# Kernel tuning notes

Hardware: AMD Instinct MI355X
Metric: run time of the kernel (lower is better)

Reference implementation:

```python
import jax, jax.numpy as jnp
from jax import lax
import numpy as np


def _conv2d(x, w, b, pad):
    # x: NCHW, w: OIHW
    o = lax.conv_general_dilated(x, w, window_strides=(1, 1),
                                 padding=[(pad, pad), (pad, pad)],
                                 dimension_numbers=('NCHW', 'OIHW', 'NCHW'))
    return o + b[None, :, None, None]


def _maxpool(x, kh, kw):
    return lax.reduce_window(x, -jnp.inf, lax.max,
                             window_dimensions=(1, 1, kh, kw),
                             window_strides=(1, 1, kh, kw),
                             padding='VALID')


def _l2norm(x, axis):
    n = jnp.sqrt(jnp.sum(x * x, axis=axis, keepdims=True))
    return x / jnp.maximum(n, 1e-12)


def setup_inputs() -> dict:
    key = jax.random.key(0)
    ks = jax.random.split(key, 12)
    d = {}
    d['x'] = jax.random.normal(ks[0], (16, 128, 40, 200), dtype=jnp.float32)
    d['cluster_centers'] = jax.random.uniform(ks[1], (64, 128), dtype=jnp.float32)
    d['conv_w'] = jax.random.normal(ks[2], (64, 128, 1, 1), dtype=jnp.float32) * 0.05
    d['conv_b'] = jax.random.normal(ks[3], (64,), dtype=jnp.float32) * 0.05
    d['w1'] = jax.random.normal(ks[4], (256, 128, 5, 5), dtype=jnp.float32) * 0.02
    d['b1'] = jax.random.normal(ks[5], (256,), dtype=jnp.float32) * 0.02
    d['w2'] = jax.random.normal(ks[6], (512, 256, 5, 5), dtype=jnp.float32) * 0.02
    d['b2'] = jax.random.normal(ks[7], (512,), dtype=jnp.float32) * 0.02
    d['w3'] = jax.random.normal(ks[8], (1024, 512, 5, 5), dtype=jnp.float32) * 0.02
    d['b3'] = jax.random.normal(ks[9], (1024,), dtype=jnp.float32) * 0.02
    d['mlp_w'] = jax.random.normal(ks[10], (256, 9216), dtype=jnp.float32) * 0.01
    d['mlp_b'] = jax.random.normal(ks[11], (256,), dtype=jnp.float32) * 0.01
    return d


def reference(x, cluster_centers, conv_w, conv_b, w1, b1, w2, b2, w3, b3, mlp_w, mlp_b):
    N, C, H, W = x.shape
    K = conv_w.shape[0]
    P = H * W

    # soft assignment: 1x1 conv -> softmax over cluster axis
    sa = _conv2d(x, conv_w, conv_b, 0).reshape(N, K, P)
    a = jax.nn.softmax(sa, axis=1)                      # [N, K, P]

    x_flat = x.reshape(N, C, P)
    # sum_p a[n,k,p] * (x[n,c,p] - centers[k,c])  -- algebraically equal to
    # the explicit NxKxCxP residual tensor, computed without materializing it.
    vlad = jnp.einsum('nkp,ncp->nkc', a, x_flat) \
           - a.sum(axis=-1)[:, :, None] * cluster_centers[None, :, :]
    vlad = _l2norm(vlad, axis=2)                        # intra-norm per cluster
    vlad = _l2norm(vlad.reshape(N, K * C), axis=1)      # [N, K*C]

    # CNN branch
    h = _conv2d(x, w1, b1, 2)
    h = jnp.where(h >= 0, h, 0.2 * h)                   # LeakyReLU(0.2)
    h = _maxpool(h, 2, 2)
    h = _conv2d(h, w2, b2, 2)
    h = jnp.where(h >= 0, h, 0.2 * h)
    h = _maxpool(h, 4, 4)
    h = _conv2d(h, w3, b3, 2)
    h = _maxpool(h, 5, 25)                              # -> [N, 1024, 1, 1]
    x_feat = _l2norm(h.reshape(N, -1), axis=1)          # [N, 1024]

    feat = jnp.concatenate([vlad, x_feat], axis=1)      # [N, 9216]
    out = feat @ mlp_w.T + mlp_b
    return _l2norm(out, axis=1)
```

## Files before the change

### kernel.cpp

```cpp
#include <hip/hip_runtime.h>
#include <math.h>

#define K_ 64
#define C_ 128
#define NB 16
#define P_ 8000

typedef float f32x4 __attribute__((ext_vector_type(4)));
typedef short s16x8 __attribute__((ext_vector_type(8)));

__device__ __forceinline__ short f2bf(float v) {
    unsigned u = __float_as_uint(v);
    u += 0x7FFFu + ((u >> 16) & 1u);
    return (short)(u >> 16);
}
__device__ __forceinline__ float bf2f(ushort u) { return __uint_as_float(((unsigned)u) << 16); }

__device__ __forceinline__ void stage16(const void* g, void* l) {
    __builtin_amdgcn_global_load_lds(
        (const __attribute__((address_space(1))) void*)g,
        (__attribute__((address_space(3))) void*)l, 16, 0, 0);
}

__global__ void k_transpose_tiled(const float* __restrict__ in, float* __restrict__ out,
                                  int Co, int E)
{
    __shared__ float t[32][33];
    const int e0  = blockIdx.x * 32;
    const int co0 = blockIdx.y * 32;
    for (int i = threadIdx.y; i < 32; i += 8) {
        int co = co0 + i, e = e0 + threadIdx.x;
        t[i][threadIdx.x] = (co < Co && e < E) ? in[(size_t)co * E + e] : 0.f;
    }
    __syncthreads();
    for (int i = threadIdx.y; i < 32; i += 8) {
        int e = e0 + i, co = co0 + threadIdx.x;
        if (e < E && co < Co) out[(size_t)e * Co + co] = t[threadIdx.x][i];
    }
}

__global__ void k_nchw_to_nhwc(const float* __restrict__ in, ushort* __restrict__ out,
                               int C, int P)
{
    __shared__ ushort t[32][33];
    const int n  = blockIdx.z;
    const int p0 = blockIdx.x * 32;
    const int c0 = blockIdx.y * 32;
    for (int i = threadIdx.y; i < 32; i += 8) {
        int c = c0 + i, p = p0 + threadIdx.x;
        t[i][threadIdx.x] = (c < C && p < P) ? (ushort)f2bf(in[((size_t)n * C + c) * P + p]) : 0;
    }
    __syncthreads();
    for (int i = threadIdx.y; i < 32; i += 8) {
        int p = p0 + i, c = c0 + threadIdx.x;
        if (p < P && c < C) out[((size_t)n * P + p) * C + c] = t[threadIdx.x][i];
    }
}

__global__ void k_wprep(const float* __restrict__ w, short* __restrict__ wb,
                        int Co, int Cin, int total)
{
    int idx = blockIdx.x * blockDim.x + threadIdx.x;
    if (idx >= total) return;
    int cl = idx & 31;
    int rest = idx >> 5;
    int co = rest % Co;
    int rest2 = rest / Co;
    int t = rest2 % 25;
    int ck = rest2 / 25;
    float v = w[((size_t)co * Cin + (ck << 5) + cl) * 25 + t];
    wb[idx] = f2bf(v);
}

template<int SR, int NC, int WR, int WC16, int IS3>
__global__ __launch_bounds__(256) void k_conv_mfma(
    const ushort* __restrict__ in, const s16x8* __restrict__ wb,
    const float* __restrict__ bias, ushort* __restrict__ outb, float* __restrict__ outf,
    const ushort* __restrict__ zg,
    int Cin, int Co, int H, int W, int WT, int leaky, int nck, int xpc, int PT)
{
    constexpr int NT   = IS3 ? 8 : (WR * WC16);
    constexpr int TOT  = SR * NC * 4;
    constexpr int TOTP = (TOT + 63) & ~63;
    __shared__ s16x8 xin[TOTP];
    __shared__ s16x8 wl[2][4][256];

    const int tid  = threadIdx.x;
    const int lane = tid & 63;
    const int wid  = tid >> 6;
    const int wm   = wid;
    const int n16  = lane & 15;
    const int g    = lane >> 4;

    const int lid  = blockIdx.x;
    const int xcd  = lid & 7;
    const int rrr  = lid >> 3;
    const int co_blk = xcd / xpc;
    const int posn = rrr * xpc + (xcd % xpc);
    const int n    = posn / PT;
    const int bx   = posn % PT;

    const int h0  = IS3 ? 0 : (bx / WT) * WR;
    const int w0  = IS3 ? 0 : (bx % WT) * (WC16 * 16);
    const int ks  = IS3 ? bx : 0;
    const int co0 = co_blk * 256;

    int ph[NT], pw[NT];
    if (IS3) {
        #pragma unroll
        for (int nt = 0; nt < NT; ++nt) {
            int pos = nt * 16 + n16;
            int h = pos / 25;
            int w = pos - h * 25;
            if (h > 4) { h = 0; w = 0; }
            ph[nt] = h; pw[nt] = w;
        }
    }

    f32x4 acc[4][NT];
    #pragma unroll
    for (int i = 0; i < 4; ++i)
        #pragma unroll
        for (int j = 0; j < NT; ++j) acc[i][j] = f32x4{0.f, 0.f, 0.f, 0.f};

    const int ck0 = IS3 ? ks * nck : 0;
    const int ckend = ck0 + nck;

    auto stage_input = [&](int ck) {
        for (int c = wid; c * 64 < TOTP; c += 4) {
            int u = c * 64 + lane;
            int row = u / (NC * 4);
            int rem = u - row * (NC * 4);
            int col = rem >> 2;
            int s   = rem & 3;
            int g8  = (s - (col >> 1) - row) & 3;
            int gh = h0 + row - 2, gw = w0 + col - 2;
            const void* src =
                (u < TOT && (unsigned)gh < (unsigned)H && (unsigned)gw < (unsigned)W)
                ? (const void*)(in + ((size_t)(n * H + gh) * W + gw) * Cin + (ck << 5) + (g8 << 3))
                : (const void*)zg;
            stage16(src, (void*)&xin[c * 64]);
        }
    };
    auto stage_w = [&](int gT, int slot) {
        const s16x8* src = wb + ((size_t)gT * Co + co0 + wm * 64) * 4 + lane;
        #pragma unroll
        for (int k = 0; k < 4; ++k)
            stage16((const void*)(src + k * 64), (void*)&wl[slot][wid][k * 64]);
    };

    for (int ck = ck0; ck < ckend; ++ck) {
        if (ck != ck0) __builtin_amdgcn_s_barrier();
        stage_input(ck);
        stage_w(ck * 25, 0);
        asm volatile("s_waitcnt vmcnt(4)" ::: "memory");
        __builtin_amdgcn_sched_barrier(0);
        __builtin_amdgcn_s_barrier();

        #pragma unroll
        for (int t = 0; t < 25; ++t) {
            if (t < 24) {
                stage_w(ck * 25 + t + 1, (t + 1) & 1);
                asm volatile("s_waitcnt vmcnt(4)" ::: "memory");
            } else {
                asm volatile("s_waitcnt vmcnt(0)" ::: "memory");
            }
            __builtin_amdgcn_sched_barrier(0);

            const int r = t / 5, s = t - (t / 5) * 5;

            const s16x8* wt_ = &wl[t & 1][wid][n16 * 4 + g];
            s16x8 wf[4];
            #pragma unroll
            for (int mt = 0; mt < 4; ++mt) wf[mt] = wt_[mt * 64];

            s16x8 bf[NT];
            #pragma unroll
            for (int nt = 0; nt < NT; ++nt) {
                int row, col;
                if (IS3) { row = ph[nt] + r; col = pw[nt] + s; }
                else {
                    int rr = nt / WC16, cc = nt - rr * WC16;
                    row = rr + r;
                    col = cc * 16 + n16 + s;
                }
                bf[nt] = xin[(row * NC + col) * 4 + ((g + (col >> 1) + row) & 3)];
            }
            __builtin_amdgcn_s_setprio(1);
            #pragma unroll
            for (int mt = 0; mt < 4; ++mt)
                #pragma unroll
                for (int nt = 0; nt < NT; ++nt)
                    acc[mt][nt] = __builtin_amdgcn_mfma_f32_16x16x32_bf16(
                        wf[mt], bf[nt], acc[mt][nt], 0, 0, 0);
            __builtin_amdgcn_s_setprio(0);
        }
    }

    if (IS3) {
        #pragma unroll
        for (int mt = 0; mt < 4; ++mt) {
            #pragma unroll
            for (int reg = 0; reg < 4; ++reg) {
                const int co = co0 + wm * 64 + mt * 16 + g * 4 + reg;
                #pragma unroll
                for (int nt = 0; nt < NT; ++nt) {
                    int pos = nt * 16 + n16;
                    if (pos < 125)
                        outf[((size_t)(ks * NB + n) * Co + co) * 125 + pos] = acc[mt][nt][reg];
                }
            }
        }
    } else {
        #pragma unroll
        for (int mt = 0; mt < 4; ++mt) {
            const int cobase = co0 + wm * 64 + mt * 16 + g * 4;
            const float b0 = bias[cobase + 0];
            const float b1 = bias[cobase + 1];
            const float b2 = bias[cobase + 2];
            const float b3 = bias[cobase + 3];
            #pragma unroll
            for (int nt = 0; nt < NT; ++nt) {
                int rr = nt / WC16, cc = nt - rr * WC16;
                int h  = h0 + rr;
                int wp = w0 + cc * 16 + n16;
                if (h < H && wp < W) {
                    float v0 = acc[mt][nt][0] + b0;
                    float v1 = acc[mt][nt][1] + b1;
                    float v2 = acc[mt][nt][2] + b2;
                    float v3 = acc[mt][nt][3] + b3;
                    if (leaky) {
                        v0 = (v0 >= 0.f) ? v0 : 0.2f * v0;
                        v1 = (v1 >= 0.f) ? v1 : 0.2f * v1;
                        v2 = (v2 >= 0.f) ? v2 : 0.2f * v2;
                        v3 = (v3 >= 0.f) ? v3 : 0.2f * v3;
                    }
                    ushort4 pkd;
                    pkd.x = (ushort)f2bf(v0);
                    pkd.y = (ushort)f2bf(v1);
                    pkd.z = (ushort)f2bf(v2);
                    pkd.w = (ushort)f2bf(v3);
                    *(ushort4*)(outb + ((size_t)(n * H + h) * W + wp) * Co + cobase) = pkd;
                }
            }
        }
    }
}

__global__ __launch_bounds__(256) void k_vlad_partial(
    const float* __restrict__ x,
    const float* __restrict__ convw_t,
    const float* __restrict__ convb,
    float* __restrict__ pv,
    float* __restrict__ pa)
{
    __shared__ float xs[C_][64];
    __shared__ float als[64][K_];
    __shared__ float pgsum[4][K_];

    const int tid = threadIdx.x;
    const int chunk = blockIdx.x;
    const int n = blockIdx.y;
    const int p0 = chunk * 64;

    const float* xn = x + (size_t)n * C_ * P_ + p0;
    for (int i = tid; i < C_ * 64; i += 256) {
        int c = i >> 6, pp = i & 63;
        xs[c][pp] = xn[(size_t)c * P_ + pp];
    }
    __syncthreads();

    const int k  = tid & 63;
    const int pg = tid >> 6;

    float sa[16];
    const float bk = convb[k];
    #pragma unroll
    for (int j = 0; j < 16; ++j) sa[j] = bk;
    for (int c = 0; c < C_; ++c) {
        float wv = convw_t[c * K_ + k];
        const float4* xp = (const float4*)&xs[c][pg * 16];
        #pragma unroll
        for (int q = 0; q < 4; ++q) {
            float4 xv = xp[q];
            sa[q*4+0] += wv * xv.x;
            sa[q*4+1] += wv * xv.y;
            sa[q*4+2] += wv * xv.z;
            sa[q*4+3] += wv * xv.w;
        }
    }

    float asum_loc = 0.f;
    #pragma unroll
    for (int j = 0; j < 16; ++j) {
        float m = sa[j];
        for (int d = 32; d >= 1; d >>= 1) m = fmaxf(m, __shfl_xor(m, d));
        float e = __expf(sa[j] - m);
        float s = e;
        for (int d = 32; d >= 1; d >>= 1) s += __shfl_xor(s, d);
        float a = e / s;
        als[pg * 16 + j][k] = a;
        asum_loc += a;
    }
    pgsum[pg][k] = asum_loc;
    __syncthreads();
    if (tid < K_) {
        pa[((size_t)n * 125 + chunk) * K_ + tid] =
            pgsum[0][tid] + pgsum[1][tid] + pgsum[2][tid] + pgsum[3][tid];
    }

    const int q = pg;
    float acc[32];
    #pragma unroll
    for (int j = 0; j < 32; ++j) acc[j] = 0.f;
    for (int p = 0; p < 64; p += 4) {
        float a0 = als[p+0][k], a1 = als[p+1][k], a2 = als[p+2][k], a3 = als[p+3][k];
        #pragma unroll
        for (int j = 0; j < 32; ++j) {
            const float4 xv = *(const float4*)&xs[q*32 + j][p];
            acc[j] += a0*xv.x + a1*xv.y + a2*xv.z + a3*xv.w;
        }
    }
    float* pvp = pv + ((((size_t)n * 125 + chunk) * K_ + k) * C_ + q * 32);
    #pragma unroll
    for (int j = 0; j < 32; ++j) pvp[j] = acc[j];
}

__global__ void k_vlad_reduce(const float* __restrict__ pv, float* __restrict__ vlad_raw)
{
    int idx = blockIdx.x * blockDim.x + threadIdx.x;
    if (idx >= NB * 8192) return;
    int n = idx >> 13;
    int rest = idx & 8191;
    const float* p = pv + (size_t)n * 125 * 8192 + rest;
    float s = 0.f;
    for (int ch = 0; ch < 125; ++ch) s += p[(size_t)ch * 8192];
    vlad_raw[(size_t)n * 8192 + rest] = s;
}

__global__ void k_asum_reduce(const float* __restrict__ pa, float* __restrict__ asum)
{
    int idx = blockIdx.x * blockDim.x + threadIdx.x;
    if (idx >= NB * K_) return;
    const float* p = pa + (size_t)(idx >> 6) * 125 * K_ + (idx & 63);
    float s = 0.f;
    for (int ch = 0; ch < 125; ++ch) s += p[ch * K_];
    asum[idx] = s;
}

__global__ __launch_bounds__(128) void k_vlad_finalize(
    const float* __restrict__ vlad_raw, const float* __restrict__ asum,
    const float* __restrict__ centers, float* __restrict__ feat)
{
    __shared__ float red[2];
    const int k = blockIdx.x, n = blockIdx.y, c = threadIdx.x;
    float v = vlad_raw[((size_t)n * K_ + k) * C_ + c] - asum[n * K_ + k] * centers[k * C_ + c];
    float ss = v * v;
    for (int d = 32; d >= 1; d >>= 1) ss += __shfl_xor(ss, d);
    if ((threadIdx.x & 63) == 0) red[threadIdx.x >> 6] = ss;
    __syncthreads();
    float denom = fmaxf(sqrtf(red[0] + red[1]), 1e-12f);
    feat[(size_t)n * 9216 + k * C_ + c] = v / denom;
}

__global__ void k_maxpool_cl(const ushort* __restrict__ in, ushort* __restrict__ out,
                             int Hi, int Wi, int C8, int ph, int pw, int total)
{
    int idx = blockIdx.x * blockDim.x + threadIdx.x;
    if (idx >= total) return;
    const int Ho = Hi / ph, Wo = Wi / pw;
    const int C = C8 << 3;
    int c8 = idx % C8;
    int t  = idx / C8;
    int wo = t % Wo; t /= Wo;
    int ho = t % Ho;
    int n  = t / Ho;
    const ushort* base = in + ((size_t)(n * Hi + ho * ph) * Wi + wo * pw) * C + (c8 << 3);
    float m[8];
    #pragma unroll
    for (int j = 0; j < 8; ++j) m[j] = -INFINITY;
    for (int r = 0; r < ph; ++r)
        for (int s = 0; s < pw; ++s) {
            s16x8 v = *(const s16x8*)(base + ((size_t)r * Wi + s) * C);
            #pragma unroll
            for (int j = 0; j < 8; ++j) m[j] = fmaxf(m[j], bf2f((ushort)v[j]));
        }
    s16x8 o;
    #pragma unroll
    for (int j = 0; j < 8; ++j) o[j] = f2bf(m[j]);
    *(s16x8*)(out + ((size_t)(n * Ho + ho) * Wo + wo) * C + (c8 << 3)) = o;
}

__global__ void k_pool3_feat(const float* __restrict__ part, const float* __restrict__ bias,
                             float* __restrict__ feat)
{
    int idx = blockIdx.x * blockDim.x + threadIdx.x;
    if (idx >= NB * 1024) return;
    int n = idx >> 10, c = idx & 1023;
    const size_t kstride = (size_t)NB * 1024 * 125;
    const float* p = part + ((size_t)n * 1024 + c) * 125;
    const float b = bias[c];
    float m = -INFINITY;
    for (int i = 0; i < 125; ++i) {
        float s = 0.f;
        #pragma unroll
        for (int ksl = 0; ksl < 8; ++ksl) s += p[i + ksl * kstride];
        m = fmaxf(m, b + s);
    }
    feat[(size_t)n * 9216 + 8192 + c] = m;
}

__global__ __launch_bounds__(256) void k_featnorm(const float* __restrict__ feat,
                                                  float* __restrict__ scale)
{
    __shared__ float r1s[4], r2s[4];
    const int n = blockIdx.x;
    const int tid = threadIdx.x;
    const int wid = tid >> 6;
    float s1 = 0.f, s2 = 0.f;
    const float* f = feat + (size_t)n * 9216;
    for (int i = tid; i < 9216; i += 256) {
        float v = f[i];
        if (i < 8192) s1 += v * v; else s2 += v * v;
    }
    for (int d = 32; d >= 1; d >>= 1) { s1 += __shfl_xor(s1, d); s2 += __shfl_xor(s2, d); }
    if ((tid & 63) == 0) { r1s[wid] = s1; r2s[wid] = s2; }
    __syncthreads();
    if (tid == 0) {
        scale[n * 2 + 0] = 1.f / fmaxf(sqrtf(r1s[0] + r1s[1] + r1s[2] + r1s[3]), 1e-12f);
        scale[n * 2 + 1] = 1.f / fmaxf(sqrtf(r2s[0] + r2s[1] + r2s[2] + r2s[3]), 1e-12f);
    }
}

__global__ __launch_bounds__(256) void k_mlp_part(
    const float* __restrict__ feat, const float* __restrict__ scale,
    const float* __restrict__ wt,
    float* __restrict__ part)
{
    __shared__ float fs[576];
    const int n  = blockIdx.x >> 4;
    const int sl = blockIdx.x & 15;
    const int tid = threadIdx.x;
    const int base = sl * 576;
    for (int j = tid; j < 576; j += 256) {
        int idx = base + j;
        fs[j] = feat[(size_t)n * 9216 + idx] * scale[n * 2 + (idx < 8192 ? 0 : 1)];
    }
    __syncthreads();
    float a0 = 0.f, a1 = 0.f;
    for (int j = 0; j < 576; j += 2) {
        a0 += fs[j]     * wt[(size_t)(base + j)     * 256 + tid];
        a1 += fs[j + 1] * wt[(size_t)(base + j + 1) * 256 + tid];
    }
    part[((size_t)n * 16 + sl) * 256 + tid] = a0 + a1;
}

__global__ __launch_bounds__(256) void k_mlp_final(
    const float* __restrict__ part, const float* __restrict__ bias,
    float* __restrict__ outp)
{
    __shared__ float red[4];
    const int n = blockIdx.x;
    const int tid = threadIdx.x;
    float a = bias[tid];
    #pragma unroll
    for (int s = 0; s < 16; ++s) a += part[((size_t)n * 16 + s) * 256 + tid];
    float ss = a * a;
    for (int d = 32; d >= 1; d >>= 1) ss += __shfl_xor(ss, d);
    if ((tid & 63) == 0) red[tid >> 6] = ss;
    __syncthreads();
    const float inv = 1.f / fmaxf(sqrtf(red[0] + red[1] + red[2] + red[3]), 1e-12f);
    outp[n * 256 + tid] = a * inv;
}

extern "C" void kernel_launch(void* const* d_in, const int* in_sizes, int n_in,
                              void* d_out, int out_size, void* d_ws, size_t ws_size,
                              hipStream_t stream)
{
    const float* x      = (const float*)d_in[0];
    const float* cents  = (const float*)d_in[1];
    const float* conv_w = (const float*)d_in[2];
    const float* conv_b = (const float*)d_in[3];
    const float* w1     = (const float*)d_in[4];
    const float* b1     = (const float*)d_in[5];
    const float* w2     = (const float*)d_in[6];
    const float* b2     = (const float*)d_in[7];
    const float* w3     = (const float*)d_in[8];
    const float* b3     = (const float*)d_in[9];
    const float* mlp_w  = (const float*)d_in[10];
    const float* mlp_b  = (const float*)d_in[11];
    float* outp = (float*)d_out;

    char* ws = (char*)d_ws;
    size_t off = 0;
    auto alloc = [&](size_t bytes) -> void* {
        off = (off + 255) & ~(size_t)255;
        void* p = ws + off;
        off += bytes;
        return p;
    };
    ushort* zguard  = (ushort*)alloc(256);
    float*  convw_t = (float*)alloc((size_t)64 * 128 * 4);
    float*  mwt     = (float*)alloc((size_t)9216 * 256 * 4);
    short*  wb1     = (short*)alloc((size_t)819200 * 2);
    short*  wb2     = (short*)alloc((size_t)3276800 * 2);
    short*  wb3     = (short*)alloc((size_t)13107200 * 2);
    ushort* x_cl    = (ushort*)alloc((size_t)NB * 8000 * 128 * 2);
    float*  vlad_raw= (float*)alloc((size_t)NB * 8192 * 4);
    float*  asum    = (float*)alloc((size_t)NB * K_ * 4);
    float*  feat    = (float*)alloc((size_t)NB * 9216 * 4);
    float*  pa      = (float*)alloc((size_t)NB * 125 * K_ * 4);
    float*  scale   = (float*)alloc((size_t)NB * 2 * 4);
    float*  mpart   = (float*)alloc((size_t)NB * 16 * 256 * 4);
    ushort* pool2b  = (ushort*)alloc((size_t)NB * 125 * 512 * 2);
    char*   slabA   = (char*)alloc((size_t)8 * NB * 1024 * 125 * 4);
    ushort* slabB   = (ushort*)alloc((size_t)NB * 2000 * 256 * 2);

    hipMemsetAsync(zguard, 0, 256, stream);

    {
        dim3 blk(32, 8);
        k_transpose_tiled<<<dim3(4, 2), blk, 0, stream>>>(conv_w, convw_t, 64, 128);
        k_transpose_tiled<<<dim3(288, 8), blk, 0, stream>>>(mlp_w, mwt, 256, 9216);
        k_wprep<<<(819200 + 255) / 256, 256, 0, stream>>>(w1, wb1, 256, 128, 819200);
        k_wprep<<<(3276800 + 255) / 256, 256, 0, stream>>>(w2, wb2, 512, 256, 3276800);
        k_wprep<<<(13107200 + 255) / 256, 256, 0, stream>>>(w3, wb3, 1024, 512, 13107200);
        k_nchw_to_nhwc<<<dim3(250, 4, NB), blk, 0, stream>>>(x, x_cl, 128, 8000);
    }

    k_vlad_partial<<<dim3(125, NB), 256, 0, stream>>>(x, convw_t, conv_b, (float*)slabA, pa);
    k_vlad_reduce<<<(NB * 8192 + 255) / 256, 256, 0, stream>>>((float*)slabA, vlad_raw);
    k_asum_reduce<<<(NB * K_ + 255) / 256, 256, 0, stream>>>(pa, asum);
    k_vlad_finalize<<<dim3(K_, NB), 128, 0, stream>>>(vlad_raw, asum, cents, feat);

    k_conv_mfma<8, 36, 4, 2, 0><<<1120, 256, 0, stream>>>(
        x_cl, (const s16x8*)wb1, b1, (ushort*)slabA, nullptr, zguard,
        128, 256, 40, 200, 7, 1, 4, 8, 70);
    {
        int tot = NB * 20 * 100 * 32;
        k_maxpool_cl<<<(tot + 255) / 256, 256, 0, stream>>>(
            (ushort*)slabA, slabB, 40, 200, 32, 2, 2, tot);
    }
    k_conv_mfma<8, 36, 4, 2, 0><<<640, 256, 0, stream>>>(
        slabB, (const s16x8*)wb2, b2, (ushort*)slabA, nullptr, zguard,
        256, 512, 20, 100, 4, 1, 8, 4, 20);
    {
        int tot = NB * 5 * 25 * 64;
        k_maxpool_cl<<<(tot + 255) / 256, 256, 0, stream>>>(
            (ushort*)slabA, pool2b, 20, 100, 64, 4, 4, tot);
    }
    k_conv_mfma<9, 29, 4, 2, 1><<<512, 256, 0, stream>>>(
        pool2b, (const s16x8*)wb3, b3, nullptr, (float*)slabA, zguard,
        512, 1024, 5, 25, 1, 0, 2, 2, 8);
    k_pool3_feat<<<(NB * 1024 + 255) / 256, 256, 0, stream>>>((float*)slabA, b3, feat);

    k_featnorm<<<NB, 256, 0, stream>>>(feat, scale);
    k_mlp_part<<<NB * 16, 256, 0, stream>>>(feat, scale, mwt, mpart);
    k_mlp_final<<<NB, 256, 0, stream>>>(mpart, mlp_b, outp);
}
```

Before: 1.141 ms.

## Load conv weights directly to registers and halve per-block tile for occupancy

The MFMA conv kernel no longer stages weights through double-buffered LDS. Each wave now reads its bf16 weight fragments straight from global memory into registers and prefetches the next tap. The spatial tile per block is halved (NT fixed to 4, fewer rows), grids are doubled, and launch bounds request 4 blocks per CU to raise occupancy. Conv3 changes its split from 8 K-slices to 4 K-slices times 2 position halves, and the pool reduction is adjusted to match. This removes LDS weight traffic and barriers, but adds redundant global weight reads across more blocks and loses the setprio hints.

```diff
diff --git a/kernel.cpp b/kernel.cpp
--- a/kernel.cpp
+++ b/kernel.cpp
@@ -73,22 +73,20 @@
 }
 
 template<int SR, int NC, int WR, int WC16, int IS3>
-__global__ __launch_bounds__(256) void k_conv_mfma(
+__global__ __launch_bounds__(256, 4) void k_conv_mfma(
     const ushort* __restrict__ in, const s16x8* __restrict__ wb,
     const float* __restrict__ bias, ushort* __restrict__ outb, float* __restrict__ outf,
     const ushort* __restrict__ zg,
     int Cin, int Co, int H, int W, int WT, int leaky, int nck, int xpc, int PT)
 {
-    constexpr int NT   = IS3 ? 8 : (WR * WC16);
+    constexpr int NT   = 4;
     constexpr int TOT  = SR * NC * 4;
     constexpr int TOTP = (TOT + 63) & ~63;
     __shared__ s16x8 xin[TOTP];
-    __shared__ s16x8 wl[2][4][256];
 
     const int tid  = threadIdx.x;
     const int lane = tid & 63;
     const int wid  = tid >> 6;
-    const int wm   = wid;
     const int n16  = lane & 15;
     const int g    = lane >> 4;
 
@@ -100,16 +98,18 @@
     const int n    = posn / PT;
     const int bx   = posn % PT;
 
-    const int h0  = IS3 ? 0 : (bx / WT) * WR;
-    const int w0  = IS3 ? 0 : (bx % WT) * (WC16 * 16);
-    const int ks  = IS3 ? bx : 0;
-    const int co0 = co_blk * 256;
+    const int h0    = IS3 ? 0 : (bx / WT) * WR;
+    const int w0    = IS3 ? 0 : (bx % WT) * (WC16 * 16);
+    const int ks    = IS3 ? (bx >> 1) : 0;
+    const int phalf = IS3 ? (bx & 1) : 0;
+    const int co0   = co_blk * 256;
+    const int cobase = co0 + wid * 64;
 
     int ph[NT], pw[NT];
     if (IS3) {
         #pragma unroll
         for (int nt = 0; nt < NT; ++nt) {
-            int pos = nt * 16 + n16;
+            int pos = phalf * 64 + nt * 16 + n16;
             int h = pos / 25;
             int w = pos - h * 25;
             if (h > 4) { h = 0; w = 0; }
@@ -142,37 +142,26 @@
             stage16(src, (void*)&xin[c * 64]);
         }
     };
-    auto stage_w = [&](int gT, int slot) {
-        const s16x8* src = wb + ((size_t)gT * Co + co0 + wm * 64) * 4 + lane;
-        #pragma unroll
-        for (int k = 0; k < 4; ++k)
-            stage16((const void*)(src + k * 64), (void*)&wl[slot][wid][k * 64]);
-    };
 
     for (int ck = ck0; ck < ckend; ++ck) {
-        if (ck != ck0) __builtin_amdgcn_s_barrier();
+        if (ck != ck0) __syncthreads();
         stage_input(ck);
-        stage_w(ck * 25, 0);
-        asm volatile("s_waitcnt vmcnt(4)" ::: "memory");
-        __builtin_amdgcn_sched_barrier(0);
-        __builtin_amdgcn_s_barrier();
+        __syncthreads();
+
+        const s16x8* wbase = wb + ((size_t)ck * 25 * Co + cobase + n16) * 4 + g;
+        s16x8 wf[4];
+        #pragma unroll
+        for (int mt = 0; mt < 4; ++mt) wf[mt] = wbase[mt * 64];
 
         #pragma unroll
         for (int t = 0; t < 25; ++t) {
+            s16x8 wfn[4];
             if (t < 24) {
-                stage_w(ck * 25 + t + 1, (t + 1) & 1);
-                asm volatile("s_waitcnt vmcnt(4)" ::: "memory");
-            } else {
-                asm volatile("s_waitcnt vmcnt(0)" ::: "memory");
+                const s16x8* wn = wbase + (size_t)(t + 1) * Co * 4;
+                #pragma unroll
+                for (int mt = 0; mt < 4; ++mt) wfn[mt] = wn[mt * 64];
             }
-            __builtin_amdgcn_sched_barrier(0);
-
             const int r = t / 5, s = t - (t / 5) * 5;
-
-            const s16x8* wt_ = &wl[t & 1][wid][n16 * 4 + g];
-            s16x8 wf[4];
-            #pragma unroll
-            for (int mt = 0; mt < 4; ++mt) wf[mt] = wt_[mt * 64];
 
             s16x8 bf[NT];
             #pragma unroll
@@ -186,14 +175,16 @@
                 }
                 bf[nt] = xin[(row * NC + col) * 4 + ((g + (col >> 1) + row) & 3)];
             }
-            __builtin_amdgcn_s_setprio(1);
             #pragma unroll
             for (int mt = 0; mt < 4; ++mt)
                 #pragma unroll
                 for (int nt = 0; nt < NT; ++nt)
                     acc[mt][nt] = __builtin_amdgcn_mfma_f32_16x16x32_bf16(
                         wf[mt], bf[nt], acc[mt][nt], 0, 0, 0);
-            __builtin_amdgcn_s_setprio(0);
+            if (t < 24) {
+                #pragma unroll
+                for (int mt = 0; mt < 4; ++mt) wf[mt] = wfn[mt];
+            }
         }
     }
 
@@ -202,10 +193,10 @@
         for (int mt = 0; mt < 4; ++mt) {
             #pragma unroll
             for (int reg = 0; reg < 4; ++reg) {
-                const int co = co0 + wm * 64 + mt * 16 + g * 4 + reg;
+                const int co = cobase + mt * 16 + g * 4 + reg;
                 #pragma unroll
                 for (int nt = 0; nt < NT; ++nt) {
-                    int pos = nt * 16 + n16;
+                    int pos = phalf * 64 + nt * 16 + n16;
                     if (pos < 125)
                         outf[((size_t)(ks * NB + n) * Co + co) * 125 + pos] = acc[mt][nt][reg];
                 }
@@ -214,11 +205,11 @@
     } else {
         #pragma unroll
         for (int mt = 0; mt < 4; ++mt) {
-            const int cobase = co0 + wm * 64 + mt * 16 + g * 4;
-            const float b0 = bias[cobase + 0];
-            const float b1 = bias[cobase + 1];
-            const float b2 = bias[cobase + 2];
-            const float b3 = bias[cobase + 3];
+            const int cb = cobase + mt * 16 + g * 4;
+            const float b0 = bias[cb + 0];
+            const float b1 = bias[cb + 1];
+            const float b2 = bias[cb + 2];
+            const float b3 = bias[cb + 3];
             #pragma unroll
             for (int nt = 0; nt < NT; ++nt) {
                 int rr = nt / WC16, cc = nt - rr * WC16;
@@ -240,7 +231,7 @@
                     pkd.y = (ushort)f2bf(v1);
                     pkd.z = (ushort)f2bf(v2);
                     pkd.w = (ushort)f2bf(v3);
-                    *(ushort4*)(outb + ((size_t)(n * H + h) * W + wp) * Co + cobase) = pkd;
+                    *(ushort4*)(outb + ((size_t)(n * H + h) * W + wp) * Co + cb) = pkd;
                 }
             }
         }
@@ -404,7 +395,7 @@
     for (int i = 0; i < 125; ++i) {
         float s = 0.f;
         #pragma unroll
-        for (int ksl = 0; ksl < 8; ++ksl) s += p[i + ksl * kstride];
+        for (int ksl = 0; ksl < 4; ++ksl) s += p[i + ksl * kstride];
         m = fmaxf(m, b + s);
     }
     feat[(size_t)n * 9216 + 8192 + c] = m;
@@ -533,25 +524,25 @@
     k_asum_reduce<<<(NB * K_ + 255) / 256, 256, 0, stream>>>(pa, asum);
     k_vlad_finalize<<<dim3(K_, NB), 128, 0, stream>>>(vlad_raw, asum, cents, feat);
 
-    k_conv_mfma<8, 36, 4, 2, 0><<<1120, 256, 0, stream>>>(
+    k_conv_mfma<6, 36, 2, 2, 0><<<2240, 256, 0, stream>>>(
         x_cl, (const s16x8*)wb1, b1, (ushort*)slabA, nullptr, zguard,
-        128, 256, 40, 200, 7, 1, 4, 8, 70);
+        128, 256, 40, 200, 7, 1, 4, 8, 140);
     {
         int tot = NB * 20 * 100 * 32;
         k_maxpool_cl<<<(tot + 255) / 256, 256, 0, stream>>>(
             (ushort*)slabA, slabB, 40, 200, 32, 2, 2, tot);
     }
-    k_conv_mfma<8, 36, 4, 2, 0><<<640, 256, 0, stream>>>(
+    k_conv_mfma<6, 36, 2, 2, 0><<<1280, 256, 0, stream>>>(
         slabB, (const s16x8*)wb2, b2, (ushort*)slabA, nullptr, zguard,
-        256, 512, 20, 100, 4, 1, 8, 4, 20);
+        256, 512, 20, 100, 4, 1, 8, 4, 40);
     {
         int tot = NB * 5 * 25 * 64;
         k_maxpool_cl<<<(tot + 255) / 256, 256, 0, stream>>>(
             (ushort*)slabA, pool2b, 20, 100, 64, 4, 4, tot);
     }
-    k_conv_mfma<9, 29, 4, 2, 1><<<512, 256, 0, stream>>>(
+    k_conv_mfma<9, 29, 2, 2, 1><<<512, 256, 0, stream>>>(
         pool2b, (const s16x8*)wb3, b3, nullptr, (float*)slabA, zguard,
-        512, 1024, 5, 25, 1, 0, 2, 2, 8);
+        512, 1024, 5, 25, 1, 0, 4, 2, 8);
     k_pool3_feat<<<(NB * 1024 + 255) / 256, 256, 0, stream>>>((float*)slabA, b3, feat);
 
     k_featnorm<<<NB, 256, 0, stream>>>(feat, scale);
```

Measured after the change: 1.868 ms. 1.64x slower.
